# Kernel optimization log

Hardware: AMD Instinct MI355X
Metric: run time of the kernel (lower is better)

## Reference

```python
import jax, jax.numpy as jnp
import numpy as np

N_EMBD = 1024
B, T = 4, 2048

def setup_inputs() -> dict:
    key = jax.random.key(0)
    k1, k2, k3, k4 = jax.random.split(key, 4)
    s = 1.0 / np.sqrt(N_EMBD)
    return {
        "x": jax.random.normal(k1, (B, T, N_EMBD), dtype=jnp.float32),
        "Wq": jax.random.normal(k2, (N_EMBD, N_EMBD), dtype=jnp.float32) * s,
        "Wk": jax.random.normal(k3, (N_EMBD, N_EMBD), dtype=jnp.float32) * s,
        "Wv": jax.random.normal(k4, (N_EMBD, N_EMBD), dtype=jnp.float32) * s,
    }

def reference(x, Wq, Wk, Wv):
    # x: [B,T,C]; torch Linear (no bias): y = x @ W.T
    Bq, Tq, C = x.shape
    q = jnp.einsum('btc,dc->btd', x, Wq)
    k = jnp.einsum('btc,dc->btd', x, Wk)
    v = jnp.einsum('btc,dc->btd', x, Wv)
    att = jnp.einsum('bqd,bkd->bqk', q, k) / jnp.sqrt(jnp.float32(C))
    causal = jnp.tril(jnp.ones((Tq, Tq), dtype=bool))  # [T,T]
    att = jnp.where(causal, att, -jnp.inf)
    w = jax.nn.softmax(att, axis=-1)
    # dropout is identity in eval mode
    out = jnp.einsum('bqk,bkd->bqd', w, v)
    return out
```

## Files before the change

### kernel.cpp

```cpp
#include <hip/hip_runtime.h>
#include <stdint.h>

typedef __attribute__((ext_vector_type(8))) __bf16 bf16x8;
typedef __attribute__((ext_vector_type(8))) unsigned short ushort8;
typedef __attribute__((ext_vector_type(4))) float f32x4;

static __device__ __forceinline__ unsigned short f2bf(float f) {
  unsigned u = __float_as_uint(f);
  u += 0x7fffu + ((u >> 16) & 1u);
  return (unsigned short)(u >> 16);
}

union U16cast { ushort8 u; bf16x8 b; };
static __device__ __forceinline__ bf16x8 as_bf16x8(ushort8 x) { U16cast t; t.u = x; return t.b; }
static __device__ __forceinline__ bf16x8 ldfrag(const unsigned short* p) {
  return as_bf16x8(*(const ushort8*)p);
}

#define GLD_LDS16(g, l)                                                        \
  __builtin_amdgcn_global_load_lds(                                            \
      (const __attribute__((address_space(1))) void*)(g),                      \
      (__attribute__((address_space(3))) void*)(l), 16, 0, 0)

__global__ __launch_bounds__(256) void cast_all(
    const float* __restrict__ x, const float* __restrict__ Wq,
    const float* __restrict__ Wk, const float* __restrict__ Wv,
    unsigned short* __restrict__ out, float* __restrict__ lzero,
    long nx4, long nw4, long n4) {
  long g = (long)blockIdx.x * blockDim.x + threadIdx.x;
  if (g < 2048) ((float4*)lzero)[g] = (float4){0.f, 0.f, 0.f, 0.f};
  long i = g;
  long stride = (long)gridDim.x * blockDim.x;
  for (; i < n4; i += stride) {
    const float4* src;
    long j = i;
    if (j < nx4) {
      src = (const float4*)x;
    } else {
      j -= nx4;
      if (j < nw4) src = (const float4*)Wq;
      else if (j < 2 * nw4) { src = (const float4*)Wk; j -= nw4; }
      else { src = (const float4*)Wv; j -= 2 * nw4; }
    }
    float4 v = src[j];
    ushort4 o;
    o.x = f2bf(v.x); o.y = f2bf(v.y); o.z = f2bf(v.z); o.w = f2bf(v.w);
    *(ushort4*)(out + i * 4) = o;
  }
}

__global__ __launch_bounds__(512, 2) void gemm_qkv(
    const unsigned short* __restrict__ A, const unsigned short* __restrict__ B,
    unsigned short* __restrict__ qkv, unsigned short* __restrict__ vT) {
  __shared__ __align__(16) unsigned short As[2][8192];
  __shared__ __align__(16) unsigned short Bs[2][12288];

  int wg = blockIdx.x;
  wg = (wg & 7) * 32 + (wg >> 3);
  const int bm = wg >> 3, bn = wg & 7;
  const int m0 = bm << 8;
  const int n0 = bn * 384;

  const int tid = threadIdx.x;

  const int srow = tid >> 2;
  const int sseg = (tid & 3) ^ ((srow >> 1) & 3);
  const unsigned short* sa = A + (long)(m0 + srow) * 1024 + sseg * 8;
  const unsigned short* sb = B + (long)(n0 + srow) * 1024 + sseg * 8;
  unsigned short* dA = &As[0][0] + tid * 8;
  unsigned short* dB = &Bs[0][0] + tid * 8;

#define STG(kt, s)                                                             \
  do {                                                                         \
    GLD_LDS16(sa + (kt) * 32, dA + (s) * 8192);                                \
    GLD_LDS16(sa + 131072 + (kt) * 32, dA + (s) * 8192 + 4096);                \
    GLD_LDS16(sb + (kt) * 32, dB + (s) * 12288);                               \
    GLD_LDS16(sb + 131072 + (kt) * 32, dB + (s) * 12288 + 4096);               \
    GLD_LDS16(sb + 262144 + (kt) * 32, dB + (s) * 12288 + 8192);               \
  } while (0)

  const int lane = tid & 63;
  const int w = tid >> 6;
  const int wrm = w >> 2;
  const int wcn = w & 3;
  const int fr = lane & 15;
  const int kb = lane >> 4;
  const int segr = (kb ^ ((fr >> 1) & 3)) << 3;
  const unsigned short* rA = &As[0][0] + (wrm * 128 + fr) * 32 + segr;
  const unsigned short* rB = &Bs[0][0] + (wcn * 96 + fr) * 32 + segr;

  f32x4 acc[8][6];
#pragma unroll
  for (int mf = 0; mf < 8; ++mf)
#pragma unroll
    for (int nf = 0; nf < 6; ++nf)
      acc[mf][nf] = (f32x4){0.f, 0.f, 0.f, 0.f};

  STG(0, 0);
  __syncthreads();

  for (int kt = 0; kt < 32; ++kt) {
    const int s = kt & 1;
    if (kt + 1 < 32) STG(kt + 1, s ^ 1);

    const unsigned short* pA = rA + s * 8192;
    const unsigned short* pB = rB + s * 12288;

    bf16x8 bv[6];
#pragma unroll
    for (int nf = 0; nf < 6; ++nf) bv[nf] = ldfrag(pB + nf * 512);

#pragma unroll
    for (int mf = 0; mf < 8; ++mf) {
      bf16x8 av = ldfrag(pA + mf * 512);
#pragma unroll
      for (int nf = 0; nf < 6; ++nf)
        acc[mf][nf] = __builtin_amdgcn_mfma_f32_16x16x32_bf16(av, bv[nf], acc[mf][nf], 0, 0, 0);
    }

    __syncthreads();
  }
#undef STG

  const int rq = kb << 2;
#pragma unroll
  for (int mf = 0; mf < 8; ++mf) {
    const int row = m0 + wrm * 128 + mf * 16 + rq;
#pragma unroll
    for (int nf = 0; nf < 6; ++nf) {
      const int colb = n0 + wcn * 96 + nf * 16;
      if (colb < 2048) {
        const int col = colb + fr;
#pragma unroll
        for (int r = 0; r < 4; ++r)
          qkv[(long)(row + r) * 3072 + col] = f2bf(acc[mf][nf][r]);
      } else {
        const int b2 = m0 >> 11;
        const int trow = (m0 & 2047) + wrm * 128 + mf * 16 + rq;
        const int colv = colb - 2048 + fr;
        ushort4 o;
        o.x = f2bf(acc[mf][nf][0]); o.y = f2bf(acc[mf][nf][1]);
        o.z = f2bf(acc[mf][nf][2]); o.w = f2bf(acc[mf][nf][3]);
        *(ushort4*)(vT + ((long)b2 * 1024 + colv) * 2048 + trow) = o;
      }
    }
  }
}

template <int MODE>
__global__ __launch_bounds__(256, 4) void gemm128(
    const unsigned short* __restrict__ A, const unsigned short* __restrict__ Bp,
    void* __restrict__ Cout, float* __restrict__ lbuf) {
  __shared__ __align__(16) unsigned short As[2][4096];
  __shared__ __align__(16) unsigned short Bs[2][4096];

  constexpr int LDA = (MODE == 1) ? 3072 : 2048;

  const int wgid = blockIdx.x;
  int m0, n0, b;
  if constexpr (MODE == 1) {
    b = wgid & 3;
    const int t = wgid >> 2;
    int bm = 0;
    while ((bm + 2) * (bm + 1) / 2 <= t) ++bm;
    const int bn = t - bm * (bm + 1) / 2;
    m0 = bm << 7; n0 = bn << 7;
  } else {
    const int xcd = wgid & 7;
    const int inner = wgid >> 3;
    const int s = inner >> 5;
    const int rem = inner & 31;
    b = rem >> 3;
    const int bn = rem & 7;
    const int bm = s ? (15 - xcd) : xcd;
    m0 = bm << 7; n0 = bn << 7;
  }

  const unsigned short* Ab = A;
  const unsigned short* Bb = Bp;
  if constexpr (MODE == 1) {
    Ab += (long)b * 2048 * 3072;
    Bb += (long)b * 2048 * 3072;
  } else {
    Ab += (long)b * 2048 * 2048;
    Bb += (long)b * 1024 * 2048;
  }

  const int tid = threadIdx.x;

  const int srow = tid >> 2;
  const int sseg = (tid & 3) ^ ((srow >> 1) & 3);
  const unsigned short* sa = Ab + (long)(m0 + srow) * LDA + sseg * 8;
  const unsigned short* sb = Bb + (long)(n0 + srow) * LDA + sseg * 8;
  const long sRj = (long)64 * LDA;
  unsigned short* dA = &As[0][0] + tid * 8;
  unsigned short* dB = &Bs[0][0] + tid * 8;

#define STG(kt, s)                                                             \
  do {                                                                         \
    GLD_LDS16(sa + (kt) * 32, dA + (s) * 4096);                                \
    GLD_LDS16(sa + sRj + (kt) * 32, dA + (s) * 4096 + 2048);                   \
    GLD_LDS16(sb + (kt) * 32, dB + (s) * 4096);                                \
    GLD_LDS16(sb + sRj + (kt) * 32, dB + (s) * 4096 + 2048);                   \
  } while (0)

  const int lane = tid & 63;
  const int w = tid >> 6;
  const int wr = w >> 1;
  const int wc = w & 1;
  const int fr = lane & 15;
  const int kb = lane >> 4;
  const unsigned short* rA0 = &As[0][0] + wr * 64 * 32;
  const unsigned short* rB0 = &Bs[0][0] + wc * 64 * 32;

  const int rq = kb << 2;

  float il[4][4];
  if constexpr (MODE == 2) {
    const float* lrow = lbuf + b * 2048;
#pragma unroll
    for (int mf = 0; mf < 4; ++mf) {
      const int row = m0 + wr * 64 + mf * 16 + rq;
#pragma unroll
      for (int r = 0; r < 4; ++r) il[mf][r] = 1.0f / lrow[row + r];
    }
  }

  f32x4 acc[4][4];
#pragma unroll
  for (int mf = 0; mf < 4; ++mf)
#pragma unroll
    for (int nf = 0; nf < 4; ++nf)
      acc[mf][nf] = (f32x4){0.f, 0.f, 0.f, 0.f};

  const int kend = (MODE == 2) ? (m0 + 128) : 1024;
  const int NT = kend >> 5;

  STG(0, 0);
  __syncthreads();

  for (int kt = 0; kt < NT; ++kt) {
    const int s = kt & 1;
    if (kt + 1 < NT) STG(kt + 1, s ^ 1);

    bf16x8 av[4], bvv[4];
#pragma unroll
    for (int mf = 0; mf < 4; ++mf) {
      const int row = mf * 16 + fr;
      const int segr = (kb ^ ((row >> 1) & 3)) << 3;
      av[mf] = ldfrag(rA0 + s * 4096 + row * 32 + segr);
    }
#pragma unroll
    for (int nf = 0; nf < 4; ++nf) {
      const int row = nf * 16 + fr;
      const int segr = (kb ^ ((row >> 1) & 3)) << 3;
      bvv[nf] = ldfrag(rB0 + s * 4096 + row * 32 + segr);
    }

#pragma unroll
    for (int mf = 0; mf < 4; ++mf)
#pragma unroll
      for (int nf = 0; nf < 4; ++nf)
        acc[mf][nf] = __builtin_amdgcn_mfma_f32_16x16x32_bf16(av[mf], bvv[nf], acc[mf][nf], 0, 0, 0);

    __syncthreads();
  }
#undef STG

  if constexpr (MODE == 1) {
    unsigned short* Pu = (unsigned short*)Cout + (long)b * 2048 * 2048;
    float* lrow = lbuf + b * 2048;
#pragma unroll
    for (int mf = 0; mf < 4; ++mf) {
      const int row = m0 + wr * 64 + mf * 16 + rq;
      float psum0 = 0.f, psum1 = 0.f, psum2 = 0.f, psum3 = 0.f;
#pragma unroll
      for (int nf = 0; nf < 4; ++nf) {
        const int col = n0 + wc * 64 + nf * 16 + fr;
        float e0 = (col > row + 0) ? 0.f : __expf(acc[mf][nf][0] * 0.03125f);
        float e1 = (col > row + 1) ? 0.f : __expf(acc[mf][nf][1] * 0.03125f);
        float e2 = (col > row + 2) ? 0.f : __expf(acc[mf][nf][2] * 0.03125f);
        float e3 = (col > row + 3) ? 0.f : __expf(acc[mf][nf][3] * 0.03125f);
        psum0 += e0; psum1 += e1; psum2 += e2; psum3 += e3;
        Pu[(long)(row + 0) * 2048 + col] = f2bf(e0);
        Pu[(long)(row + 1) * 2048 + col] = f2bf(e1);
        Pu[(long)(row + 2) * 2048 + col] = f2bf(e2);
        Pu[(long)(row + 3) * 2048 + col] = f2bf(e3);
      }
#pragma unroll
      for (int off = 1; off < 16; off <<= 1) {
        psum0 += __shfl_xor(psum0, off);
        psum1 += __shfl_xor(psum1, off);
        psum2 += __shfl_xor(psum2, off);
        psum3 += __shfl_xor(psum3, off);
      }
      if (fr == 0) {
        atomicAdd(&lrow[row + 0], psum0);
        atomicAdd(&lrow[row + 1], psum1);
        atomicAdd(&lrow[row + 2], psum2);
        atomicAdd(&lrow[row + 3], psum3);
      }
    }
  } else {
    float* Cf = (float*)Cout + (long)b * 2048 * 1024;
#pragma unroll
    for (int mf = 0; mf < 4; ++mf) {
      const int row = m0 + wr * 64 + mf * 16 + rq;
#pragma unroll
      for (int nf = 0; nf < 4; ++nf) {
        const int col = n0 + wc * 64 + nf * 16 + fr;
        Cf[(long)(row + 0) * 1024 + col] = acc[mf][nf][0] * il[mf][0];
        Cf[(long)(row + 1) * 1024 + col] = acc[mf][nf][1] * il[mf][1];
        Cf[(long)(row + 2) * 1024 + col] = acc[mf][nf][2] * il[mf][2];
        Cf[(long)(row + 3) * 1024 + col] = acc[mf][nf][3] * il[mf][3];
      }
    }
  }
}

extern "C" void kernel_launch(void* const* d_in, const int* in_sizes, int n_in,
                              void* d_out, int out_size, void* d_ws, size_t ws_size,
                              hipStream_t stream) {
  const float* x  = (const float*)d_in[0];
  const float* Wq = (const float*)d_in[1];
  const float* Wk = (const float*)d_in[2];
  const float* Wv = (const float*)d_in[3];
  float* out = (float*)d_out;

  const int Bb = 4, T = 2048, C = 1024;
  const long BT = (long)Bb * T;
  const int N3 = 3 * C;

  char* ws = (char*)d_ws;
  unsigned short* xb   = (unsigned short*)ws; ws += BT * C * 2;
  unsigned short* wbuf = (unsigned short*)ws; ws += (long)N3 * C * 2;
  unsigned short* qkv  = (unsigned short*)ws; ws += BT * N3 * 2;
  unsigned short* vT   = (unsigned short*)ws; ws += BT * C * 2;
  unsigned short* Pu   = (unsigned short*)ws; ws += (long)Bb * T * T * 2;
  float* lbuf          = (float*)ws;          ws += BT * 4;

  const long nx4 = BT * C / 4, nw4 = (long)C * C / 4;
  cast_all<<<2048, 256, 0, stream>>>(x, Wq, Wk, Wv, xb, lbuf, nx4, nw4, nx4 + 3 * nw4);

  gemm_qkv<<<dim3(256, 1, 1), 512, 0, stream>>>(xb, wbuf, qkv, vT);

  gemm128<1><<<dim3(544, 1, 1), 256, 0, stream>>>(qkv, qkv + C, Pu, lbuf);

  gemm128<2><<<dim3(512, 1, 1), 256, 0, stream>>>(Pu, vT, out, lbuf);
}
```

Before: 153.5 us.

## Triple-buffer QKV GEMM with four-phase interleaved LDS loads and MFMA clusters

```diff
diff --git a/kernel.cpp b/kernel.cpp
--- a/kernel.cpp
+++ b/kernel.cpp
@@ -16,6 +16,8 @@
 static __device__ __forceinline__ bf16x8 ldfrag(const unsigned short* p) {
   return as_bf16x8(*(const ushort8*)p);
 }
+
+#define MFMA16(a, b, c) __builtin_amdgcn_mfma_f32_16x16x32_bf16((a), (b), (c), 0, 0, 0)
 
 #define GLD_LDS16(g, l)                                                        \
   __builtin_amdgcn_global_load_lds(                                            \
@@ -52,8 +54,8 @@
 __global__ __launch_bounds__(512, 2) void gemm_qkv(
     const unsigned short* __restrict__ A, const unsigned short* __restrict__ B,
     unsigned short* __restrict__ qkv, unsigned short* __restrict__ vT) {
-  __shared__ __align__(16) unsigned short As[2][8192];
-  __shared__ __align__(16) unsigned short Bs[2][12288];
+  __shared__ __align__(16) unsigned short As[3][8192];
+  __shared__ __align__(16) unsigned short Bs[3][12288];
 
   int wg = blockIdx.x;
   wg = (wg & 7) * 32 + (wg >> 3);
@@ -70,14 +72,11 @@
   unsigned short* dA = &As[0][0] + tid * 8;
   unsigned short* dB = &Bs[0][0] + tid * 8;
 
-#define STG(kt, s)                                                             \
-  do {                                                                         \
-    GLD_LDS16(sa + (kt) * 32, dA + (s) * 8192);                                \
-    GLD_LDS16(sa + 131072 + (kt) * 32, dA + (s) * 8192 + 4096);                \
-    GLD_LDS16(sb + (kt) * 32, dB + (s) * 12288);                               \
-    GLD_LDS16(sb + 131072 + (kt) * 32, dB + (s) * 12288 + 4096);               \
-    GLD_LDS16(sb + 262144 + (kt) * 32, dB + (s) * 12288 + 8192);               \
-  } while (0)
+#define SA0(kt, bu) GLD_LDS16(sa + (kt) * 32,          dA + (bu) * 8192)
+#define SA1(kt, bu) GLD_LDS16(sa + 131072 + (kt) * 32, dA + (bu) * 8192 + 4096)
+#define SB0(kt, bu) GLD_LDS16(sb + (kt) * 32,          dB + (bu) * 12288)
+#define SB1(kt, bu) GLD_LDS16(sb + 131072 + (kt) * 32, dB + (bu) * 12288 + 4096)
+#define SB2(kt, bu) GLD_LDS16(sb + 262144 + (kt) * 32, dB + (bu) * 12288 + 8192)
 
   const int lane = tid & 63;
   const int w = tid >> 6;
@@ -96,31 +95,89 @@
     for (int nf = 0; nf < 6; ++nf)
       acc[mf][nf] = (f32x4){0.f, 0.f, 0.f, 0.f};
 
-  STG(0, 0);
-  __syncthreads();
-
+  SA0(0, 0); SA1(0, 0); SB0(0, 0); SB1(0, 0); SB2(0, 0);
+  SA0(1, 1); SA1(1, 1); SB0(1, 1); SB1(1, 1); SB2(1, 1);
+  asm volatile("s_waitcnt vmcnt(5)" ::: "memory");
+  __builtin_amdgcn_s_barrier();
+  __builtin_amdgcn_sched_barrier(0);
+
+  int c0 = 0, c2 = 2;
+#pragma unroll 1
   for (int kt = 0; kt < 32; ++kt) {
-    const int s = kt & 1;
-    if (kt + 1 < 32) STG(kt + 1, s ^ 1);
-
-    const unsigned short* pA = rA + s * 8192;
-    const unsigned short* pB = rB + s * 12288;
-
-    bf16x8 bv[6];
-#pragma unroll
-    for (int nf = 0; nf < 6; ++nf) bv[nf] = ldfrag(pB + nf * 512);
-
-#pragma unroll
-    for (int mf = 0; mf < 8; ++mf) {
-      bf16x8 av = ldfrag(pA + mf * 512);
-#pragma unroll
-      for (int nf = 0; nf < 6; ++nf)
-        acc[mf][nf] = __builtin_amdgcn_mfma_f32_16x16x32_bf16(av, bv[nf], acc[mf][nf], 0, 0, 0);
-    }
-
-    __syncthreads();
-  }
-#undef STG
+    const unsigned short* pA = rA + c0 * 8192;
+    const unsigned short* pB = rB + c0 * 12288;
+    const int k2 = kt + 2;
+    const bool st = (kt < 30);
+    bf16x8 a[4], b0v[3], b1v[3];
+
+#pragma unroll
+    for (int mf = 0; mf < 4; ++mf) a[mf] = ldfrag(pA + mf * 512);
+#pragma unroll
+    for (int nf = 0; nf < 3; ++nf) b0v[nf] = ldfrag(pB + nf * 512);
+    if (st) { SA0(k2, c2); SA1(k2, c2); }
+    __builtin_amdgcn_s_barrier();
+    asm volatile("s_waitcnt lgkmcnt(0)" ::: "memory");
+    __builtin_amdgcn_sched_barrier(0);
+    __builtin_amdgcn_s_setprio(1);
+#pragma unroll
+    for (int mf = 0; mf < 4; ++mf)
+#pragma unroll
+      for (int nf = 0; nf < 3; ++nf)
+        acc[mf][nf] = MFMA16(a[mf], b0v[nf], acc[mf][nf]);
+    __builtin_amdgcn_s_setprio(0);
+    __builtin_amdgcn_s_barrier();
+
+#pragma unroll
+    for (int nf = 0; nf < 3; ++nf) b1v[nf] = ldfrag(pB + (3 + nf) * 512);
+    if (st) { SB0(k2, c2); SB1(k2, c2); }
+    __builtin_amdgcn_s_barrier();
+    asm volatile("s_waitcnt lgkmcnt(0)" ::: "memory");
+    __builtin_amdgcn_sched_barrier(0);
+    __builtin_amdgcn_s_setprio(1);
+#pragma unroll
+    for (int mf = 0; mf < 4; ++mf)
+#pragma unroll
+      for (int nf = 0; nf < 3; ++nf)
+        acc[mf][3 + nf] = MFMA16(a[mf], b1v[nf], acc[mf][3 + nf]);
+    __builtin_amdgcn_s_setprio(0);
+    __builtin_amdgcn_s_barrier();
+
+#pragma unroll
+    for (int mf = 0; mf < 4; ++mf) a[mf] = ldfrag(pA + 2048 + mf * 512);
+    if (st) SB2(k2, c2);
+    __builtin_amdgcn_s_barrier();
+    asm volatile("s_waitcnt lgkmcnt(0)" ::: "memory");
+    __builtin_amdgcn_sched_barrier(0);
+    __builtin_amdgcn_s_setprio(1);
+#pragma unroll
+    for (int mf = 0; mf < 4; ++mf)
+#pragma unroll
+      for (int nf = 0; nf < 3; ++nf)
+        acc[4 + mf][nf] = MFMA16(a[mf], b0v[nf], acc[4 + mf][nf]);
+    __builtin_amdgcn_s_setprio(0);
+    __builtin_amdgcn_s_barrier();
+
+    if (kt <= 29)      asm volatile("s_waitcnt vmcnt(5)" ::: "memory");
+    else if (kt == 30) asm volatile("s_waitcnt vmcnt(0)" ::: "memory");
+    __builtin_amdgcn_s_barrier();
+    __builtin_amdgcn_sched_barrier(0);
+    __builtin_amdgcn_s_setprio(1);
+#pragma unroll
+    for (int mf = 0; mf < 4; ++mf)
+#pragma unroll
+      for (int nf = 0; nf < 3; ++nf)
+        acc[4 + mf][3 + nf] = MFMA16(a[mf], b1v[nf], acc[4 + mf][3 + nf]);
+    __builtin_amdgcn_s_setprio(0);
+    __builtin_amdgcn_s_barrier();
+
+    c0 = (c0 == 2) ? 0 : c0 + 1;
+    c2 = (c2 == 2) ? 0 : c2 + 1;
+  }
+#undef SA0
+#undef SA1
+#undef SB0
+#undef SB1
+#undef SB2
 
   const int rq = kb << 2;
 #pragma unroll
@@ -261,7 +318,7 @@
     for (int mf = 0; mf < 4; ++mf)
 #pragma unroll
       for (int nf = 0; nf < 4; ++nf)
-        acc[mf][nf] = __builtin_amdgcn_mfma_f32_16x16x32_bf16(av[mf], bvv[nf], acc[mf][nf], 0, 0, 0);
+        acc[mf][nf] = MFMA16(av[mf], bvv[nf], acc[mf][nf]);
 
     __syncthreads();
   }
```

New measurement: 149.5 us, median of 2. 2.6% less time.
